# Optimization experiments

Measured on AMD Instinct MI355X. Metric: run time of the kernel, lower is better.

The kernel has to match this reference:

```python
import jax, jax.numpy as jnp
import numpy as np

B, N, C = 8, 4096, 768
H = 12
D = C // H            # 64
BN = C // 2           # bottleneck dim 384
EPS_LN = 1e-5
EPS_ATTN = 1e-6


def layer_norm(x, g, b):
    mu = jnp.mean(x, axis=-1, keepdims=True)
    var = jnp.mean(jnp.square(x - mu), axis=-1, keepdims=True)
    return (x - mu) * jax.lax.rsqrt(var + EPS_LN) * g + b


def setup_inputs() -> dict:
    key = jax.random.key(0)
    ks = jax.random.split(key, 8)
    s = 0.02
    return {
        "x": jax.random.normal(ks[0], (B, N, C), jnp.float32),
        "w_qkv": jax.random.normal(ks[1], (C, 3 * C), jnp.float32) * s,
        "b_qkv": jnp.zeros((3 * C,), jnp.float32),
        "w_proj": jax.random.normal(ks[2], (C, C), jnp.float32) * s,
        "b_proj": jnp.zeros((C,), jnp.float32),
        "g1": jnp.ones((C,), jnp.float32),
        "beta1": jnp.zeros((C,), jnp.float32),
        "g2": jnp.ones((C,), jnp.float32),
        "beta2": jnp.zeros((C,), jnp.float32),
        "w_down": jax.random.normal(ks[3], (C, BN), jnp.float32) * s,
        "b_down": jnp.zeros((BN,), jnp.float32),
        "w_up": jax.random.normal(ks[4], (BN, C), jnp.float32) * s,
        "b_up": jnp.zeros((C,), jnp.float32),
        "g3": jnp.ones((C,), jnp.float32),
        "beta3": jnp.zeros((C,), jnp.float32),
    }


def _linear_attention(x, w_qkv, b_qkv, w_proj, b_proj):
    # x: (B, N, C)
    qkv = x @ w_qkv + b_qkv                       # (B, N, 3C)
    qkv = qkv.reshape(B, N, 3, H, D)
    qkv = jnp.transpose(qkv, (2, 0, 3, 1, 4))     # (3, B, H, N, D)
    q, k, v = qkv[0], qkv[1], qkv[2]
    fm = lambda t: jax.nn.elu(t) + 1.0            # positive feature map
    q, k = fm(q), fm(k)
    kv = jnp.einsum('bhnd,bhnv->bhdv', k, v)      # (B, H, D, D)
    out = jnp.einsum('bhnd,bhdv->bhnv', q, kv)    # (B, H, N, D)
    k_sum = k.sum(axis=2)                         # (B, H, D)
    normalizer = jnp.einsum('bhnd,bhd->bhn', q, k_sum) + EPS_ATTN
    out = out / normalizer[..., None]
    out = jnp.transpose(out, (0, 2, 1, 3)).reshape(B, N, C)
    return out @ w_proj + b_proj


def reference(x, w_qkv, b_qkv, w_proj, b_proj, g1, beta1, g2, beta2,
              w_down, b_down, w_up, b_up, g3, beta3):
    # DinomalyBlock forward (eval mode: dropout/noise disabled)
    x = x + _linear_attention(layer_norm(x, g1, beta1), w_qkv, b_qkv, w_proj, b_proj)
    r = layer_norm(x, g2, beta2)
    h = jax.nn.gelu(r @ w_down + b_down, approximate=False)  # torch GELU default = exact
    h = h @ w_up + b_up
    return layer_norm(r + h, g3, beta3)
```

## Files before the change

kernel.cpp:

```cpp
#include <hip/hip_runtime.h>
#include <hip/hip_bf16.h>
#include <cstdio>


typedef __attribute__((ext_vector_type(8))) short short8;
typedef __attribute__((ext_vector_type(4))) float floatx4;

__device__ __forceinline__ float bf2f(unsigned short u) {
    return __uint_as_float(((unsigned int)u) << 16);
}
__device__ __forceinline__ unsigned short f2bf(float f) {
    __hip_bfloat16 h = __float2bfloat16(f);
    return *reinterpret_cast<unsigned short*>(&h);
}

__device__ __forceinline__ void async_copy16(const unsigned short* g, unsigned short* l) {
    __builtin_amdgcn_global_load_lds(
        (const __attribute__((address_space(1))) unsigned int*)g,
        (__attribute__((address_space(3))) unsigned int*)l, 16, 0, 0);
}

__device__ __forceinline__ floatx4 MFMA16(short8 a, short8 b, floatx4 c) {
    return __builtin_amdgcn_mfma_f32_16x16x32_bf16(a, b, c, 0, 0, 0);
}

__global__ __launch_bounds__(256) void transpose_all(
    const float* __restrict__ wq, const float* __restrict__ wp,
    const float* __restrict__ wd, const float* __restrict__ wu,
    unsigned short* __restrict__ tq, unsigned short* __restrict__ tp,
    unsigned short* __restrict__ td, unsigned short* __restrict__ tu)
{
    int blk = blockIdx.x;
    const float* w; unsigned short* o; int K, Nc, tx32;
    if (blk < 1728)      { w = wq; o = tq; K = 768; Nc = 2304; tx32 = 24; }
    else if (blk < 2304) { w = wp; o = tp; K = 768; Nc = 768;  tx32 = 24; blk -= 1728; }
    else if (blk < 2592) { w = wd; o = td; K = 768; Nc = 384;  tx32 = 24; blk -= 2304; }
    else                 { w = wu; o = tu; K = 384; Nc = 768;  tx32 = 12; blk -= 2592; }
    int kb = (blk % tx32) * 32, nb = (blk / tx32) * 32;
    __shared__ float tile[32][33];
    int tx = threadIdx.x & 31, ty = threadIdx.x >> 5;
    #pragma unroll
    for (int i = 0; i < 32; i += 8)
        tile[ty + i][tx] = w[(size_t)(kb + ty + i) * Nc + nb + tx];
    __syncthreads();
    #pragma unroll
    for (int i = 0; i < 32; i += 8)
        o[(size_t)(nb + ty + i) * K + kb + tx] = f2bf(tile[tx][ty + i]);
}

template<bool OBF16>
__global__ __launch_bounds__(384) void ln_kernel(
    const float* __restrict__ in, const float* __restrict__ gw,
    const float* __restrict__ bw, void* __restrict__ outp)
{
    int row = blockIdx.x;
    int t = threadIdx.x;
    float2 xv = ((const float2*)(in + (size_t)row * 768))[t];
    float s = xv.x + xv.y;
    float ss = xv.x * xv.x + xv.y * xv.y;
    #pragma unroll
    for (int o = 32; o > 0; o >>= 1) {
        s += __shfl_down(s, o);
        ss += __shfl_down(ss, o);
    }
    __shared__ float red[14];
    int wave = t >> 6, lane = t & 63;
    if (lane == 0) { red[wave] = s; red[6 + wave] = ss; }
    __syncthreads();
    if (t == 0) {
        float S = 0.f, SS = 0.f;
        #pragma unroll
        for (int i = 0; i < 6; i++) { S += red[i]; SS += red[6 + i]; }
        float mu = S * (1.0f / 768.0f);
        float var = SS * (1.0f / 768.0f) - mu * mu;
        red[12] = mu;
        red[13] = rsqrtf(var + 1e-5f);
    }
    __syncthreads();
    float mu = red[12], rstd = red[13];
    float2 g = ((const float2*)gw)[t];
    float2 b = ((const float2*)bw)[t];
    float y0 = (xv.x - mu) * rstd * g.x + b.x;
    float y1 = (xv.y - mu) * rstd * g.y + b.y;
    if (OBF16) {
        unsigned int pk = (unsigned int)f2bf(y0) | ((unsigned int)f2bf(y1) << 16);
        ((unsigned int*)outp)[(size_t)row * 384 + t] = pk;
    } else {
        ((float2*)outp)[(size_t)row * 384 + t] = make_float2(y0, y1);
    }
}

template<bool RES_F32, bool OUT_F32>
__global__ __launch_bounds__(384) void add_ln_kernel(
    const unsigned short* __restrict__ y, const void* __restrict__ resv,
    const float* __restrict__ gw, const float* __restrict__ bw,
    void* __restrict__ outp)
{
    int row = blockIdx.x;
    int t = threadIdx.x;
    unsigned int yp = ((const unsigned int*)(y + (size_t)row * 768))[t];
    float a0 = bf2f((unsigned short)(yp & 0xffff));
    float a1 = bf2f((unsigned short)(yp >> 16));
    float r0, r1;
    if (RES_F32) {
        float2 rv = ((const float2*)((const float*)resv + (size_t)row * 768))[t];
        r0 = rv.x; r1 = rv.y;
    } else {
        unsigned int rp = ((const unsigned int*)((const unsigned short*)resv + (size_t)row * 768))[t];
        r0 = bf2f((unsigned short)(rp & 0xffff));
        r1 = bf2f((unsigned short)(rp >> 16));
    }
    float v0 = a0 + r0, v1 = a1 + r1;
    float s = v0 + v1;
    float ss = v0 * v0 + v1 * v1;
    #pragma unroll
    for (int o = 32; o > 0; o >>= 1) {
        s += __shfl_down(s, o);
        ss += __shfl_down(ss, o);
    }
    __shared__ float red[14];
    int wave = t >> 6, lane = t & 63;
    if (lane == 0) { red[wave] = s; red[6 + wave] = ss; }
    __syncthreads();
    if (t == 0) {
        float S = 0.f, SS = 0.f;
        #pragma unroll
        for (int i = 0; i < 6; i++) { S += red[i]; SS += red[6 + i]; }
        float mu = S * (1.0f / 768.0f);
        float var = SS * (1.0f / 768.0f) - mu * mu;
        red[12] = mu;
        red[13] = rsqrtf(var + 1e-5f);
    }
    __syncthreads();
    float mu = red[12], rstd = red[13];
    float2 g = ((const float2*)gw)[t];
    float2 b = ((const float2*)bw)[t];
    float y0 = (v0 - mu) * rstd * g.x + b.x;
    float y1 = (v1 - mu) * rstd * g.y + b.y;
    if (OUT_F32) {
        ((float2*)outp)[(size_t)row * 384 + t] = make_float2(y0, y1);
    } else {
        unsigned int pk = (unsigned int)f2bf(y0) | ((unsigned int)f2bf(y1) << 16);
        ((unsigned int*)outp)[(size_t)row * 384 + t] = pk;
    }
}

template<int MODE>
__global__ __launch_bounds__(256, 4) void gemm_kernel(
    const unsigned short* __restrict__ A,
    const unsigned short* __restrict__ Wt,
    const float* __restrict__ bias,
    unsigned short* __restrict__ outp,
    int M, int K, int Nc)
{
    __shared__ __align__(16) unsigned short As[128][64];
    __shared__ __align__(16) unsigned short Bs[128][64];

    const int gx = gridDim.x;
    const int gy = gridDim.y;
    int rb, cb;
    {
        const int lid = blockIdx.y * gx + blockIdx.x;
        const int xcd = lid & 7;
        const int o   = lid >> 3;
        const int pry = gy >> 3;
        const int cpg = (gx >= 12) ? (gx >> 1) : gx;
        const int per = pry * cpg;
        const int grp = o / per;
        const int o2  = o - grp * per;
        rb = xcd * pry + o2 / cpg;
        cb = grp * cpg + o2 % cpg;
    }
    const int row0 = rb * 128;
    const int col0 = cb * 128;

    const int t = threadIdx.x;
    const int lane = t & 63;
    const int wave = t >> 6;
    const int wm = (wave >> 1) * 64;
    const int wn = (wave & 1) * 64;
    const int frow = lane & 15;
    const int quad = lane >> 4;
    const int lrow = lane >> 3;
    const int lchunk = (lane & 7) ^ lrow;

    floatx4 acc[4][4];
    #pragma unroll
    for (int i = 0; i < 4; i++)
        #pragma unroll
        for (int j = 0; j < 4; j++)
            acc[i][j] = (floatx4){0.f, 0.f, 0.f, 0.f};

    for (int k0 = 0; k0 < K; k0 += 64) {
        __syncthreads();
        #pragma unroll
        for (int q = 0; q < 4; q++) {
            int r = wave * 32 + q * 8 + lrow;
            async_copy16(A  + (size_t)(row0 + r) * K + k0 + lchunk * 8, &As[wave * 32 + q * 8][0]);
            async_copy16(Wt + (size_t)(col0 + r) * K + k0 + lchunk * 8, &Bs[wave * 32 + q * 8][0]);
        }
        __syncthreads();
        #pragma unroll
        for (int ks = 0; ks < 2; ks++) {
            const int pc = ((ks * 4 + quad) ^ (frow & 7)) * 8;
            short8 af[4], bf4[4];
            #pragma unroll
            for (int i = 0; i < 4; i++) af[i] = *(const short8*)&As[wm + i * 16 + frow][pc];
            #pragma unroll
            for (int j = 0; j < 4; j++) bf4[j] = *(const short8*)&Bs[wn + j * 16 + frow][pc];
            #pragma unroll
            for (int i = 0; i < 4; i++)
                #pragma unroll
                for (int j = 0; j < 4; j++)
                    acc[i][j] = MFMA16(af[i], bf4[j], acc[i][j]);
        }
    }

    #pragma unroll
    for (int i = 0; i < 4; i++) {
        #pragma unroll
        for (int j = 0; j < 4; j++) {
            int col = col0 + wn + j * 16 + frow;
            float bcol = bias[col];
            #pragma unroll
            for (int rr = 0; rr < 4; rr++) {
                int row = row0 + wm + i * 16 + quad * 4 + rr;
                float v = acc[i][j][rr] + bcol;
                if (MODE == 0) {
                    if (col < 1536) v = (v > 0.f) ? (v + 1.f) : expf(v);
                } else if (MODE == 2) {
                    v = 0.5f * v * (1.0f + erff(v * 0.70710678118654752f));
                }
                outp[(size_t)row * Nc + col] = f2bf(v);
            }
        }
    }
}

__global__ __launch_bounds__(256, 4) void kv_accum(
    const unsigned short* __restrict__ qkv, float* __restrict__ kvbuf)
{
    int blk = blockIdx.x;
    int chunk = blk & 7;
    int bh = blk >> 3;
    int b = bh / 12, h = bh % 12;
    int n0 = chunk * 512;
    int t = threadIdx.x;
    int d = t & 63, g = t >> 6;
    __shared__ float kl[32][68];
    __shared__ float vl[32][68];
    float kv[16];
    #pragma unroll
    for (int j = 0; j < 16; j++) kv[j] = 0.f;
    float ks = 0.f;

    int sr = t >> 3;
    int c16 = (t & 7) * 16;
    bool isk = c16 < 64;
    int cc = isk ? c16 : c16 - 64;
    const unsigned short* gbase =
        qkv + (size_t)(b * 4096 + n0 + sr) * 2304 + (isk ? 768 : 1536) + h * 64 + cc;
    uint4 r0, r1;
    auto loadg = [&](int nb) {
        const uint4* s = (const uint4*)(gbase + (size_t)nb * 2304);
        r0 = s[0]; r1 = s[1];
    };
    auto storel = [&]() {
        float* dst = isk ? &kl[sr][cc] : &vl[sr][cc];
        const unsigned short* u0 = (const unsigned short*)&r0;
        const unsigned short* u1 = (const unsigned short*)&r1;
        #pragma unroll
        for (int i = 0; i < 8; i++) dst[i] = bf2f(u0[i]);
        #pragma unroll
        for (int i = 0; i < 8; i++) dst[8 + i] = bf2f(u1[i]);
    };

    loadg(0);
    for (int c = 0; c < 16; c++) {
        storel();
        __syncthreads();
        if (c < 15) loadg((c + 1) * 32);
        #pragma unroll 8
        for (int r2 = 0; r2 < 32; r2++) {
            float kd = kl[r2][d];
            ks += kd;
            const float4* vv = (const float4*)&vl[r2][g * 16];
            float4 a0 = vv[0], a1 = vv[1], a2 = vv[2], a3 = vv[3];
            kv[0]  += kd * a0.x; kv[1]  += kd * a0.y; kv[2]  += kd * a0.z; kv[3]  += kd * a0.w;
            kv[4]  += kd * a1.x; kv[5]  += kd * a1.y; kv[6]  += kd * a1.z; kv[7]  += kd * a1.w;
            kv[8]  += kd * a2.x; kv[9]  += kd * a2.y; kv[10] += kd * a2.z; kv[11] += kd * a2.w;
            kv[12] += kd * a3.x; kv[13] += kd * a3.y; kv[14] += kd * a3.z; kv[15] += kd * a3.w;
        }
        __syncthreads();
    }
    float* dstg = kvbuf + (size_t)bh * 4160;
    #pragma unroll
    for (int j = 0; j < 16; j++)
        atomicAdd(&dstg[(g * 16 + j) * 64 + d], kv[j]);
    if (g == 0) atomicAdd(&dstg[4096 + d], ks);
}

__global__ __launch_bounds__(256) void attn_apply(
    const unsigned short* __restrict__ qkv, const float* __restrict__ kvbuf,
    unsigned short* __restrict__ attnC)
{
    int blk = blockIdx.x;
    int nchunk = blk & 31;
    int bh = blk >> 5;
    int b = bh / 12, h = bh % 12;
    int n0 = nchunk * 128;
    int t = threadIdx.x;
    int lane = t & 63, wave = t >> 6;
    __shared__ __align__(16) unsigned short ql[128][72];
    __shared__ __align__(16) unsigned short Bs[80][72];

    {
        const float* kvg = kvbuf + (size_t)bh * 4160;
        int e = t >> 2, d0 = (t & 3) * 16;
        const float4* src4 = (const float4*)(kvg + e * 64 + d0);
        #pragma unroll
        for (int i = 0; i < 4; i++) {
            float4 v = src4[i];
            unsigned long long pk = (unsigned long long)f2bf(v.x)
                | ((unsigned long long)f2bf(v.y) << 16)
                | ((unsigned long long)f2bf(v.z) << 32)
                | ((unsigned long long)f2bf(v.w) << 48);
            *(unsigned long long*)&Bs[e][d0 + i * 4] = pk;
        }
        if (t < 64) {
            Bs[64][t] = f2bf(kvg[4096 + t]);
            #pragma unroll
            for (int r = 65; r < 80; r++) Bs[r][t] = 0;
        }
    }
    {
        int r = t >> 1, c0 = (t & 1) * 32;
        const uint4* src = (const uint4*)(qkv + (size_t)(b * 4096 + n0 + r) * 2304 + h * 64 + c0);
        uint4* dst = (uint4*)&ql[r][c0];
        #pragma unroll
        for (int i = 0; i < 4; i++) dst[i] = src[i];
    }
    __syncthreads();

    int frow = lane & 15, quad = lane >> 4;
    floatx4 acc[2][5];
    #pragma unroll
    for (int it = 0; it < 2; it++)
        #pragma unroll
        for (int jt = 0; jt < 5; jt++)
            acc[it][jt] = (floatx4){0.f, 0.f, 0.f, 0.f};

    #pragma unroll
    for (int ks = 0; ks < 2; ks++) {
        int fk = ks * 32 + quad * 8;
        short8 a0 = *(const short8*)&ql[wave * 32 + frow][fk];
        short8 a1 = *(const short8*)&ql[wave * 32 + 16 + frow][fk];
        #pragma unroll
        for (int jt = 0; jt < 5; jt++) {
            short8 bb = *(const short8*)&Bs[jt * 16 + frow][fk];
            acc[0][jt] = __builtin_amdgcn_mfma_f32_16x16x32_bf16(a0, bb, acc[0][jt], 0, 0, 0);
            acc[1][jt] = __builtin_amdgcn_mfma_f32_16x16x32_bf16(a1, bb, acc[1][jt], 0, 0, 0);
        }
    }

    #pragma unroll
    for (int it = 0; it < 2; it++) {
        #pragma unroll
        for (int rr = 0; rr < 4; rr++) {
            float nv = __shfl(acc[it][4][rr], (lane & 48));
            float inv = 1.0f / (nv + 1e-6f);
            int row = n0 + wave * 32 + it * 16 + quad * 4 + rr;
            size_t obase = (size_t)(b * 4096 + row) * 768 + h * 64;
            #pragma unroll
            for (int jt = 0; jt < 4; jt++)
                attnC[obase + jt * 16 + frow] = f2bf(acc[it][jt][rr] * inv);
        }
    }
}

extern "C" void kernel_launch(void* const* d_in, const int* in_sizes, int n_in,
                              void* d_out, int out_size, void* d_ws, size_t ws_size,
                              hipStream_t stream)
{
    const float* x      = (const float*)d_in[0];
    const float* w_qkv  = (const float*)d_in[1];
    const float* b_qkv  = (const float*)d_in[2];
    const float* w_proj = (const float*)d_in[3];
    const float* b_proj = (const float*)d_in[4];
    const float* g1     = (const float*)d_in[5];
    const float* be1    = (const float*)d_in[6];
    const float* g2     = (const float*)d_in[7];
    const float* be2    = (const float*)d_in[8];
    const float* w_down = (const float*)d_in[9];
    const float* b_down = (const float*)d_in[10];
    const float* w_up   = (const float*)d_in[11];
    const float* b_up   = (const float*)d_in[12];
    const float* g3     = (const float*)d_in[13];
    const float* be3    = (const float*)d_in[14];

    char* p = (char*)d_ws;
    auto take = [&](size_t b) { char* q = p; p += (b + 255) & ~(size_t)255; return q; };
    unsigned short* wtq  = (unsigned short*)take((size_t)2304 * 768 * 2);
    unsigned short* wtp  = (unsigned short*)take((size_t)768 * 768 * 2);
    unsigned short* wtd  = (unsigned short*)take((size_t)384 * 768 * 2);
    unsigned short* wtu  = (unsigned short*)take((size_t)768 * 384 * 2);
    unsigned short* bufA = (unsigned short*)take((size_t)32768 * 768 * 2);
    unsigned short* qkvb = (unsigned short*)take((size_t)32768 * 2304 * 2);
    float*          kvb  = (float*)take((size_t)96 * 4160 * 4);
    unsigned short* hbuf = (unsigned short*)take((size_t)32768 * 384 * 2);
    unsigned short* rbuf    = qkvb;
    unsigned short* projout = qkvb + (size_t)32768 * 768;
    unsigned short* upout   = qkvb + (size_t)2 * 32768 * 768;

    size_t needed = (size_t)(p - (char*)d_ws);
    if (needed > ws_size)
        fprintf(stderr, "WARNING: ws too small: need %zu have %zu\n", needed, ws_size);

    transpose_all<<<2880, 256, 0, stream>>>(w_qkv, w_proj, w_down, w_up, wtq, wtp, wtd, wtu);
    hipMemsetAsync(kvb, 0, (size_t)96 * 4160 * 4, stream);

    ln_kernel<true><<<32768, 384, 0, stream>>>(x, g1, be1, bufA);
    gemm_kernel<0><<<dim3(18, 256), 256, 0, stream>>>(bufA, wtq, b_qkv, qkvb, 32768, 768, 2304);
    kv_accum<<<768, 256, 0, stream>>>(qkvb, kvb);
    attn_apply<<<3072, 256, 0, stream>>>(qkvb, kvb, bufA);
    gemm_kernel<1><<<dim3(6, 256), 256, 0, stream>>>(bufA, wtp, b_proj, projout, 32768, 768, 768);
    add_ln_kernel<true, false><<<32768, 384, 0, stream>>>(projout, x, g2, be2, rbuf);
    gemm_kernel<2><<<dim3(3, 256), 256, 0, stream>>>(rbuf, wtd, b_down, hbuf, 32768, 768, 384);
    gemm_kernel<1><<<dim3(6, 256), 256, 0, stream>>>(hbuf, wtu, b_up, upout, 32768, 384, 768);
    add_ln_kernel<false, true><<<32768, 384, 0, stream>>>(upout, rbuf, g3, be3, (float*)d_out);
}
```

Baseline: 649.1 us.

## Process two rows per LayerNorm block with float4 loads; drop GEMM block swizzle

The LayerNorm and add+LayerNorm kernels now handle two rows per 384-thread block, each thread loading four elements with float4 or uint2 accesses, which halves the block count and widens the memory transactions. Separately, the GEMM kernel drops its XCD-aware block-index remapping and uses plain blockIdx tiling. The wider loads should cut per-block overhead in the bandwidth-bound LN kernels. Removing the swizzle may hurt L2 locality for the GEMMs on the multi-XCD chip.

After: 646.6 us. Within noise of the previous version (-0.4%).

```diff
diff --git a/kernel.cpp b/kernel.cpp
--- a/kernel.cpp
+++ b/kernel.cpp
@@ -53,40 +53,46 @@
     const float* __restrict__ in, const float* __restrict__ gw,
     const float* __restrict__ bw, void* __restrict__ outp)
 {
-    int row = blockIdx.x;
     int t = threadIdx.x;
-    float2 xv = ((const float2*)(in + (size_t)row * 768))[t];
-    float s = xv.x + xv.y;
-    float ss = xv.x * xv.x + xv.y * xv.y;
+    int half = (t >= 192) ? 1 : 0;
+    int tt = t - half * 192;
+    int row = blockIdx.x * 2 + half;
+    float4 xv = ((const float4*)(in + (size_t)row * 768))[tt];
+    float s = xv.x + xv.y + xv.z + xv.w;
+    float ss = xv.x * xv.x + xv.y * xv.y + xv.z * xv.z + xv.w * xv.w;
     #pragma unroll
     for (int o = 32; o > 0; o >>= 1) {
         s += __shfl_down(s, o);
         ss += __shfl_down(ss, o);
     }
-    __shared__ float red[14];
+    __shared__ float red[16];
     int wave = t >> 6, lane = t & 63;
-    if (lane == 0) { red[wave] = s; red[6 + wave] = ss; }
-    __syncthreads();
-    if (t == 0) {
-        float S = 0.f, SS = 0.f;
-        #pragma unroll
-        for (int i = 0; i < 6; i++) { S += red[i]; SS += red[6 + i]; }
+    if (lane == 0) { red[wave] = s; red[8 + wave] = ss; }
+    __syncthreads();
+    if (tt == 0) {
+        int w0 = half * 3;
+        float S = red[w0] + red[w0 + 1] + red[w0 + 2];
+        float SS = red[8 + w0] + red[8 + w0 + 1] + red[8 + w0 + 2];
         float mu = S * (1.0f / 768.0f);
         float var = SS * (1.0f / 768.0f) - mu * mu;
-        red[12] = mu;
-        red[13] = rsqrtf(var + 1e-5f);
-    }
-    __syncthreads();
-    float mu = red[12], rstd = red[13];
-    float2 g = ((const float2*)gw)[t];
-    float2 b = ((const float2*)bw)[t];
+        red[6 + half] = mu;
+        red[14 + half] = rsqrtf(var + 1e-5f);
+    }
+    __syncthreads();
+    float mu = red[6 + half], rstd = red[14 + half];
+    float4 g = ((const float4*)gw)[tt];
+    float4 b = ((const float4*)bw)[tt];
     float y0 = (xv.x - mu) * rstd * g.x + b.x;
     float y1 = (xv.y - mu) * rstd * g.y + b.y;
+    float y2 = (xv.z - mu) * rstd * g.z + b.z;
+    float y3 = (xv.w - mu) * rstd * g.w + b.w;
     if (OBF16) {
-        unsigned int pk = (unsigned int)f2bf(y0) | ((unsigned int)f2bf(y1) << 16);
-        ((unsigned int*)outp)[(size_t)row * 384 + t] = pk;
+        uint2 pk;
+        pk.x = (unsigned int)f2bf(y0) | ((unsigned int)f2bf(y1) << 16);
+        pk.y = (unsigned int)f2bf(y2) | ((unsigned int)f2bf(y3) << 16);
+        ((uint2*)outp)[(size_t)row * 192 + tt] = pk;
     } else {
-        ((float2*)outp)[(size_t)row * 384 + t] = make_float2(y0, y1);
+        ((float4*)outp)[(size_t)row * 192 + tt] = make_float4(y0, y1, y2, y3);
     }
 }
 
@@ -96,52 +102,62 @@
     const float* __restrict__ gw, const float* __restrict__ bw,
     void* __restrict__ outp)
 {
-    int row = blockIdx.x;
     int t = threadIdx.x;
-    unsigned int yp = ((const unsigned int*)(y + (size_t)row * 768))[t];
-    float a0 = bf2f((unsigned short)(yp & 0xffff));
-    float a1 = bf2f((unsigned short)(yp >> 16));
-    float r0, r1;
+    int half = (t >= 192) ? 1 : 0;
+    int tt = t - half * 192;
+    int row = blockIdx.x * 2 + half;
+    uint2 yp = ((const uint2*)(y + (size_t)row * 768))[tt];
+    float a0 = bf2f((unsigned short)(yp.x & 0xffff));
+    float a1 = bf2f((unsigned short)(yp.x >> 16));
+    float a2 = bf2f((unsigned short)(yp.y & 0xffff));
+    float a3 = bf2f((unsigned short)(yp.y >> 16));
+    float r0, r1, r2, r3;
     if (RES_F32) {
-        float2 rv = ((const float2*)((const float*)resv + (size_t)row * 768))[t];
-        r0 = rv.x; r1 = rv.y;
+        float4 rv = ((const float4*)((const float*)resv + (size_t)row * 768))[tt];
+        r0 = rv.x; r1 = rv.y; r2 = rv.z; r3 = rv.w;
     } else {
-        unsigned int rp = ((const unsigned int*)((const unsigned short*)resv + (size_t)row * 768))[t];
-        r0 = bf2f((unsigned short)(rp & 0xffff));
-        r1 = bf2f((unsigned short)(rp >> 16));
-    }
-    float v0 = a0 + r0, v1 = a1 + r1;
-    float s = v0 + v1;
-    float ss = v0 * v0 + v1 * v1;
+        uint2 rp = ((const uint2*)((const unsigned short*)resv + (size_t)row * 768))[tt];
+        r0 = bf2f((unsigned short)(rp.x & 0xffff));
+        r1 = bf2f((unsigned short)(rp.x >> 16));
+        r2 = bf2f((unsigned short)(rp.y & 0xffff));
+        r3 = bf2f((unsigned short)(rp.y >> 16));
+    }
+    float v0 = a0 + r0, v1 = a1 + r1, v2 = a2 + r2, v3 = a3 + r3;
+    float s = v0 + v1 + v2 + v3;
+    float ss = v0 * v0 + v1 * v1 + v2 * v2 + v3 * v3;
     #pragma unroll
     for (int o = 32; o > 0; o >>= 1) {
         s += __shfl_down(s, o);
         ss += __shfl_down(ss, o);
     }
-    __shared__ float red[14];
+    __shared__ float red[16];
     int wave = t >> 6, lane = t & 63;
-    if (lane == 0) { red[wave] = s; red[6 + wave] = ss; }
-    __syncthreads();
-    if (t == 0) {
-        float S = 0.f, SS = 0.f;
-        #pragma unroll
-        for (int i = 0; i < 6; i++) { S += red[i]; SS += red[6 + i]; }
+    if (lane == 0) { red[wave] = s; red[8 + wave] = ss; }
+    __syncthreads();
+    if (tt == 0) {
+        int w0 = half * 3;
+        float S = red[w0] + red[w0 + 1] + red[w0 + 2];
+        float SS = red[8 + w0] + red[8 + w0 + 1] + red[8 + w0 + 2];
         float mu = S * (1.0f / 768.0f);
         float var = SS * (1.0f / 768.0f) - mu * mu;
-        red[12] = mu;
-        red[13] = rsqrtf(var + 1e-5f);
-    }
-    __syncthreads();
-    float mu = red[12], rstd = red[13];
-    float2 g = ((const float2*)gw)[t];
-    float2 b = ((const float2*)bw)[t];
+        red[6 + half] = mu;
+        red[14 + half] = rsqrtf(var + 1e-5f);
+    }
+    __syncthreads();
+    float mu = red[6 + half], rstd = red[14 + half];
+    float4 g = ((const float4*)gw)[tt];
+    float4 b = ((const float4*)bw)[tt];
     float y0 = (v0 - mu) * rstd * g.x + b.x;
     float y1 = (v1 - mu) * rstd * g.y + b.y;
+    float y2 = (v2 - mu) * rstd * g.z + b.z;
+    float y3 = (v3 - mu) * rstd * g.w + b.w;
     if (OUT_F32) {
-        ((float2*)outp)[(size_t)row * 384 + t] = make_float2(y0, y1);
+        ((float4*)outp)[(size_t)row * 192 + tt] = make_float4(y0, y1, y2, y3);
     } else {
-        unsigned int pk = (unsigned int)f2bf(y0) | ((unsigned int)f2bf(y1) << 16);
-        ((unsigned int*)outp)[(size_t)row * 384 + t] = pk;
+        uint2 pk;
+        pk.x = (unsigned int)f2bf(y0) | ((unsigned int)f2bf(y1) << 16);
+        pk.y = (unsigned int)f2bf(y2) | ((unsigned int)f2bf(y3) << 16);
+        ((uint2*)outp)[(size_t)row * 192 + tt] = pk;
     }
 }
 
@@ -155,25 +171,8 @@
 {
     __shared__ __align__(16) unsigned short As[128][64];
     __shared__ __align__(16) unsigned short Bs[128][64];
-
-    const int gx = gridDim.x;
-    const int gy = gridDim.y;
-    int rb, cb;
-    {
-        const int lid = blockIdx.y * gx + blockIdx.x;
-        const int xcd = lid & 7;
-        const int o   = lid >> 3;
-        const int pry = gy >> 3;
-        const int cpg = (gx >= 12) ? (gx >> 1) : gx;
-        const int per = pry * cpg;
-        const int grp = o / per;
-        const int o2  = o - grp * per;
-        rb = xcd * pry + o2 / cpg;
-        cb = grp * cpg + o2 % cpg;
-    }
-    const int row0 = rb * 128;
-    const int col0 = cb * 128;
-
+    const int row0 = blockIdx.y * 128;
+    const int col0 = blockIdx.x * 128;
     const int t = threadIdx.x;
     const int lane = t & 63;
     const int wave = t >> 6;
@@ -419,13 +418,13 @@
     transpose_all<<<2880, 256, 0, stream>>>(w_qkv, w_proj, w_down, w_up, wtq, wtp, wtd, wtu);
     hipMemsetAsync(kvb, 0, (size_t)96 * 4160 * 4, stream);
 
-    ln_kernel<true><<<32768, 384, 0, stream>>>(x, g1, be1, bufA);
+    ln_kernel<true><<<16384, 384, 0, stream>>>(x, g1, be1, bufA);
     gemm_kernel<0><<<dim3(18, 256), 256, 0, stream>>>(bufA, wtq, b_qkv, qkvb, 32768, 768, 2304);
     kv_accum<<<768, 256, 0, stream>>>(qkvb, kvb);
     attn_apply<<<3072, 256, 0, stream>>>(qkvb, kvb, bufA);
     gemm_kernel<1><<<dim3(6, 256), 256, 0, stream>>>(bufA, wtp, b_proj, projout, 32768, 768, 768);
-    add_ln_kernel<true, false><<<32768, 384, 0, stream>>>(projout, x, g2, be2, rbuf);
+    add_ln_kernel<true, false><<<16384, 384, 0, stream>>>(projout, x, g2, be2, rbuf);
     gemm_kernel<2><<<dim3(3, 256), 256, 0, stream>>>(rbuf, wtd, b_down, hbuf, 32768, 768, 384);
     gemm_kernel<1><<<dim3(6, 256), 256, 0, stream>>>(hbuf, wtu, b_up, upout, 32768, 384, 768);
-    add_ln_kernel<false, true><<<32768, 384, 0, stream>>>(upout, rbuf, g3, be3, (float*)d_out);
-}
+    add_ln_kernel<false, true><<<16384, 384, 0, stream>>>(upout, rbuf, g3, be3, (float*)d_out);
+}
```

## Use wave-per-row layernorms, drop GEMM XCD swizzle, stage attention output via LDS

Applied to the files above, without the earlier changes.

The layernorm and add-layernorm kernels now assign one wavefront per row, with four rows per 256-thread block. They use float4/uint2 vector loads and a shuffle-xor reduction, so the LDS round trip and both block barriers go away. The GEMM drops its XCD-aware block remapping and uses plain blockIdx tiling, which may reduce L2 locality across chiplets. The attention-apply epilogue writes results into LDS first and then stores them with coalesced 16-byte global writes instead of scattered 2-byte stores.

New measurement: 611.9 us. -5.7%, faster.

```diff
diff --git a/kernel.cpp b/kernel.cpp
--- a/kernel.cpp
+++ b/kernel.cpp
@@ -49,99 +49,127 @@
 }
 
 template<bool OBF16>
-__global__ __launch_bounds__(384) void ln_kernel(
+__global__ __launch_bounds__(256) void ln_kernel(
     const float* __restrict__ in, const float* __restrict__ gw,
     const float* __restrict__ bw, void* __restrict__ outp)
 {
-    int row = blockIdx.x;
     int t = threadIdx.x;
-    float2 xv = ((const float2*)(in + (size_t)row * 768))[t];
-    float s = xv.x + xv.y;
-    float ss = xv.x * xv.x + xv.y * xv.y;
-    #pragma unroll
-    for (int o = 32; o > 0; o >>= 1) {
-        s += __shfl_down(s, o);
-        ss += __shfl_down(ss, o);
-    }
-    __shared__ float red[14];
-    int wave = t >> 6, lane = t & 63;
-    if (lane == 0) { red[wave] = s; red[6 + wave] = ss; }
-    __syncthreads();
-    if (t == 0) {
-        float S = 0.f, SS = 0.f;
-        #pragma unroll
-        for (int i = 0; i < 6; i++) { S += red[i]; SS += red[6 + i]; }
-        float mu = S * (1.0f / 768.0f);
-        float var = SS * (1.0f / 768.0f) - mu * mu;
-        red[12] = mu;
-        red[13] = rsqrtf(var + 1e-5f);
-    }
-    __syncthreads();
-    float mu = red[12], rstd = red[13];
-    float2 g = ((const float2*)gw)[t];
-    float2 b = ((const float2*)bw)[t];
-    float y0 = (xv.x - mu) * rstd * g.x + b.x;
-    float y1 = (xv.y - mu) * rstd * g.y + b.y;
+    int lane = t & 63, wave = t >> 6;
+    int row = blockIdx.x * 4 + wave;
+    const float4* src = (const float4*)(in + (size_t)row * 768);
+    float4 x0 = src[lane], x1 = src[lane + 64], x2 = src[lane + 128];
+    float s  = (x0.x + x0.y + x0.z + x0.w)
+             + (x1.x + x1.y + x1.z + x1.w)
+             + (x2.x + x2.y + x2.z + x2.w);
+    float ss = (x0.x * x0.x + x0.y * x0.y + x0.z * x0.z + x0.w * x0.w)
+             + (x1.x * x1.x + x1.y * x1.y + x1.z * x1.z + x1.w * x1.w)
+             + (x2.x * x2.x + x2.y * x2.y + x2.z * x2.z + x2.w * x2.w);
+    #pragma unroll
+    for (int o = 1; o < 64; o <<= 1) {
+        s += __shfl_xor(s, o);
+        ss += __shfl_xor(ss, o);
+    }
+    float mu = s * (1.0f / 768.0f);
+    float var = ss * (1.0f / 768.0f) - mu * mu;
+    float rstd = rsqrtf(var + 1e-5f);
+    float4 g0 = ((const float4*)gw)[lane], g1 = ((const float4*)gw)[lane + 64],
+           g2 = ((const float4*)gw)[lane + 128];
+    float4 b0 = ((const float4*)bw)[lane], b1 = ((const float4*)bw)[lane + 64],
+           b2 = ((const float4*)bw)[lane + 128];
+    float4 y0, y1, y2;
+    y0.x = (x0.x - mu) * rstd * g0.x + b0.x; y0.y = (x0.y - mu) * rstd * g0.y + b0.y;
+    y0.z = (x0.z - mu) * rstd * g0.z + b0.z; y0.w = (x0.w - mu) * rstd * g0.w + b0.w;
+    y1.x = (x1.x - mu) * rstd * g1.x + b1.x; y1.y = (x1.y - mu) * rstd * g1.y + b1.y;
+    y1.z = (x1.z - mu) * rstd * g1.z + b1.z; y1.w = (x1.w - mu) * rstd * g1.w + b1.w;
+    y2.x = (x2.x - mu) * rstd * g2.x + b2.x; y2.y = (x2.y - mu) * rstd * g2.y + b2.y;
+    y2.z = (x2.z - mu) * rstd * g2.z + b2.z; y2.w = (x2.w - mu) * rstd * g2.w + b2.w;
     if (OBF16) {
-        unsigned int pk = (unsigned int)f2bf(y0) | ((unsigned int)f2bf(y1) << 16);
-        ((unsigned int*)outp)[(size_t)row * 384 + t] = pk;
+        uint2* dst = (uint2*)outp + (size_t)row * 192;
+        uint2 p0, p1, p2;
+        p0.x = (unsigned int)f2bf(y0.x) | ((unsigned int)f2bf(y0.y) << 16);
+        p0.y = (unsigned int)f2bf(y0.z) | ((unsigned int)f2bf(y0.w) << 16);
+        p1.x = (unsigned int)f2bf(y1.x) | ((unsigned int)f2bf(y1.y) << 16);
+        p1.y = (unsigned int)f2bf(y1.z) | ((unsigned int)f2bf(y1.w) << 16);
+        p2.x = (unsigned int)f2bf(y2.x) | ((unsigned int)f2bf(y2.y) << 16);
+        p2.y = (unsigned int)f2bf(y2.z) | ((unsigned int)f2bf(y2.w) << 16);
+        dst[lane] = p0; dst[lane + 64] = p1; dst[lane + 128] = p2;
     } else {
-        ((float2*)outp)[(size_t)row * 384 + t] = make_float2(y0, y1);
+        float4* dst = (float4*)outp + (size_t)row * 192;
+        dst[lane] = y0; dst[lane + 64] = y1; dst[lane + 128] = y2;
     }
 }
 
 template<bool RES_F32, bool OUT_F32>
-__global__ __launch_bounds__(384) void add_ln_kernel(
+__global__ __launch_bounds__(256) void add_ln_kernel(
     const unsigned short* __restrict__ y, const void* __restrict__ resv,
     const float* __restrict__ gw, const float* __restrict__ bw,
     void* __restrict__ outp)
 {
-    int row = blockIdx.x;
     int t = threadIdx.x;
-    unsigned int yp = ((const unsigned int*)(y + (size_t)row * 768))[t];
-    float a0 = bf2f((unsigned short)(yp & 0xffff));
-    float a1 = bf2f((unsigned short)(yp >> 16));
-    float r0, r1;
+    int lane = t & 63, wave = t >> 6;
+    int row = blockIdx.x * 4 + wave;
+    const uint2* ysrc = (const uint2*)(y + (size_t)row * 768);
+    uint2 ya = ysrc[lane], yb = ysrc[lane + 64], yc = ysrc[lane + 128];
+    float v[12];
+    v[0] = bf2f((unsigned short)(ya.x & 0xffff)); v[1] = bf2f((unsigned short)(ya.x >> 16));
+    v[2] = bf2f((unsigned short)(ya.y & 0xffff)); v[3] = bf2f((unsigned short)(ya.y >> 16));
+    v[4] = bf2f((unsigned short)(yb.x & 0xffff)); v[5] = bf2f((unsigned short)(yb.x >> 16));
+    v[6] = bf2f((unsigned short)(yb.y & 0xffff)); v[7] = bf2f((unsigned short)(yb.y >> 16));
+    v[8] = bf2f((unsigned short)(yc.x & 0xffff)); v[9] = bf2f((unsigned short)(yc.x >> 16));
+    v[10] = bf2f((unsigned short)(yc.y & 0xffff)); v[11] = bf2f((unsigned short)(yc.y >> 16));
     if (RES_F32) {
-        float2 rv = ((const float2*)((const float*)resv + (size_t)row * 768))[t];
-        r0 = rv.x; r1 = rv.y;
+        const float4* rsrc = (const float4*)((const float*)resv + (size_t)row * 768);
+        float4 r0 = rsrc[lane], r1 = rsrc[lane + 64], r2 = rsrc[lane + 128];
+        v[0] += r0.x; v[1] += r0.y; v[2] += r0.z; v[3] += r0.w;
+        v[4] += r1.x; v[5] += r1.y; v[6] += r1.z; v[7] += r1.w;
+        v[8] += r2.x; v[9] += r2.y; v[10] += r2.z; v[11] += r2.w;
     } else {
-        unsigned int rp = ((const unsigned int*)((const unsigned short*)resv + (size_t)row * 768))[t];
-        r0 = bf2f((unsigned short)(rp & 0xffff));
-        r1 = bf2f((unsigned short)(rp >> 16));
-    }
-    float v0 = a0 + r0, v1 = a1 + r1;
-    float s = v0 + v1;
-    float ss = v0 * v0 + v1 * v1;
-    #pragma unroll
-    for (int o = 32; o > 0; o >>= 1) {
-        s += __shfl_down(s, o);
-        ss += __shfl_down(ss, o);
-    }
-    __shared__ float red[14];
-    int wave = t >> 6, lane = t & 63;
-    if (lane == 0) { red[wave] = s; red[6 + wave] = ss; }
-    __syncthreads();
-    if (t == 0) {
-        float S = 0.f, SS = 0.f;
-        #pragma unroll
-        for (int i = 0; i < 6; i++) { S += red[i]; SS += red[6 + i]; }
-        float mu = S * (1.0f / 768.0f);
-        float var = SS * (1.0f / 768.0f) - mu * mu;
-        red[12] = mu;
-        red[13] = rsqrtf(var + 1e-5f);
-    }
-    __syncthreads();
-    float mu = red[12], rstd = red[13];
-    float2 g = ((const float2*)gw)[t];
-    float2 b = ((const float2*)bw)[t];
-    float y0 = (v0 - mu) * rstd * g.x + b.x;
-    float y1 = (v1 - mu) * rstd * g.y + b.y;
+        const uint2* rsrc = (const uint2*)((const unsigned short*)resv + (size_t)row * 768);
+        uint2 r0 = rsrc[lane], r1 = rsrc[lane + 64], r2 = rsrc[lane + 128];
+        v[0] += bf2f((unsigned short)(r0.x & 0xffff)); v[1] += bf2f((unsigned short)(r0.x >> 16));
+        v[2] += bf2f((unsigned short)(r0.y & 0xffff)); v[3] += bf2f((unsigned short)(r0.y >> 16));
+        v[4] += bf2f((unsigned short)(r1.x & 0xffff)); v[5] += bf2f((unsigned short)(r1.x >> 16));
+        v[6] += bf2f((unsigned short)(r1.y & 0xffff)); v[7] += bf2f((unsigned short)(r1.y >> 16));
+        v[8] += bf2f((unsigned short)(r2.x & 0xffff)); v[9] += bf2f((unsigned short)(r2.x >> 16));
+        v[10] += bf2f((unsigned short)(r2.y & 0xffff)); v[11] += bf2f((unsigned short)(r2.y >> 16));
+    }
+    float s = 0.f, ss = 0.f;
+    #pragma unroll
+    for (int i = 0; i < 12; i++) { s += v[i]; ss += v[i] * v[i]; }
+    #pragma unroll
+    for (int o = 1; o < 64; o <<= 1) {
+        s += __shfl_xor(s, o);
+        ss += __shfl_xor(ss, o);
+    }
+    float mu = s * (1.0f / 768.0f);
+    float var = ss * (1.0f / 768.0f) - mu * mu;
+    float rstd = rsqrtf(var + 1e-5f);
+    float4 g0 = ((const float4*)gw)[lane], g1 = ((const float4*)gw)[lane + 64],
+           g2 = ((const float4*)gw)[lane + 128];
+    float4 b0 = ((const float4*)bw)[lane], b1 = ((const float4*)bw)[lane + 64],
+           b2 = ((const float4*)bw)[lane + 128];
+    float yv[12];
+    yv[0] = (v[0] - mu) * rstd * g0.x + b0.x; yv[1] = (v[1] - mu) * rstd * g0.y + b0.y;
+    yv[2] = (v[2] - mu) * rstd * g0.z + b0.z; yv[3] = (v[3] - mu) * rstd * g0.w + b0.w;
+    yv[4] = (v[4] - mu) * rstd * g1.x + b1.x; yv[5] = (v[5] - mu) * rstd * g1.y + b1.y;
+    yv[6] = (v[6] - mu) * rstd * g1.z + b1.z; yv[7] = (v[7] - mu) * rstd * g1.w + b1.w;
+    yv[8] = (v[8] - mu) * rstd * g2.x + b2.x; yv[9] = (v[9] - mu) * rstd * g2.y + b2.y;
+    yv[10] = (v[10] - mu) * rstd * g2.z + b2.z; yv[11] = (v[11] - mu) * rstd * g2.w + b2.w;
     if (OUT_F32) {
-        ((float2*)outp)[(size_t)row * 384 + t] = make_float2(y0, y1);
+        float4* dst = (float4*)outp + (size_t)row * 192;
+        dst[lane] = make_float4(yv[0], yv[1], yv[2], yv[3]);
+        dst[lane + 64] = make_float4(yv[4], yv[5], yv[6], yv[7]);
+        dst[lane + 128] = make_float4(yv[8], yv[9], yv[10], yv[11]);
     } else {
-        unsigned int pk = (unsigned int)f2bf(y0) | ((unsigned int)f2bf(y1) << 16);
-        ((unsigned int*)outp)[(size_t)row * 384 + t] = pk;
+        uint2* dst = (uint2*)outp + (size_t)row * 192;
+        uint2 p0, p1, p2;
+        p0.x = (unsigned int)f2bf(yv[0]) | ((unsigned int)f2bf(yv[1]) << 16);
+        p0.y = (unsigned int)f2bf(yv[2]) | ((unsigned int)f2bf(yv[3]) << 16);
+        p1.x = (unsigned int)f2bf(yv[4]) | ((unsigned int)f2bf(yv[5]) << 16);
+        p1.y = (unsigned int)f2bf(yv[6]) | ((unsigned int)f2bf(yv[7]) << 16);
+        p2.x = (unsigned int)f2bf(yv[8]) | ((unsigned int)f2bf(yv[9]) << 16);
+        p2.y = (unsigned int)f2bf(yv[10]) | ((unsigned int)f2bf(yv[11]) << 16);
+        dst[lane] = p0; dst[lane + 64] = p1; dst[lane + 128] = p2;
     }
 }
 
@@ -155,25 +183,8 @@
 {
     __shared__ __align__(16) unsigned short As[128][64];
     __shared__ __align__(16) unsigned short Bs[128][64];
-
-    const int gx = gridDim.x;
-    const int gy = gridDim.y;
-    int rb, cb;
-    {
-        const int lid = blockIdx.y * gx + blockIdx.x;
-        const int xcd = lid & 7;
-        const int o   = lid >> 3;
-        const int pry = gy >> 3;
-        const int cpg = (gx >= 12) ? (gx >> 1) : gx;
-        const int per = pry * cpg;
-        const int grp = o / per;
-        const int o2  = o - grp * per;
-        rb = xcd * pry + o2 / cpg;
-        cb = grp * cpg + o2 % cpg;
-    }
-    const int row0 = rb * 128;
-    const int col0 = cb * 128;
-
+    const int row0 = blockIdx.y * 128;
+    const int col0 = blockIdx.x * 128;
     const int t = threadIdx.x;
     const int lane = t & 63;
     const int wave = t >> 6;
@@ -369,12 +380,20 @@
         for (int rr = 0; rr < 4; rr++) {
             float nv = __shfl(acc[it][4][rr], (lane & 48));
             float inv = 1.0f / (nv + 1e-6f);
-            int row = n0 + wave * 32 + it * 16 + quad * 4 + rr;
-            size_t obase = (size_t)(b * 4096 + row) * 768 + h * 64;
+            int lr = it * 16 + quad * 4 + rr;
             #pragma unroll
             for (int jt = 0; jt < 4; jt++)
-                attnC[obase + jt * 16 + frow] = f2bf(acc[it][jt][rr] * inv);
-        }
+                ql[wave * 32 + lr][jt * 16 + frow] = f2bf(acc[it][jt][rr] * inv);
+        }
+    }
+    #pragma unroll
+    for (int j = 0; j < 4; j++) {
+        int u = j * 64 + lane;
+        int lr = u >> 3;
+        int c8 = (u & 7) * 8;
+        uint4 val = *(const uint4*)&ql[wave * 32 + lr][c8];
+        int row = n0 + wave * 32 + lr;
+        *(uint4*)&attnC[(size_t)(b * 4096 + row) * 768 + h * 64 + c8] = val;
     }
 }
 
@@ -419,13 +438,13 @@
     transpose_all<<<2880, 256, 0, stream>>>(w_qkv, w_proj, w_down, w_up, wtq, wtp, wtd, wtu);
     hipMemsetAsync(kvb, 0, (size_t)96 * 4160 * 4, stream);
 
-    ln_kernel<true><<<32768, 384, 0, stream>>>(x, g1, be1, bufA);
+    ln_kernel<true><<<8192, 256, 0, stream>>>(x, g1, be1, bufA);
     gemm_kernel<0><<<dim3(18, 256), 256, 0, stream>>>(bufA, wtq, b_qkv, qkvb, 32768, 768, 2304);
     kv_accum<<<768, 256, 0, stream>>>(qkvb, kvb);
     attn_apply<<<3072, 256, 0, stream>>>(qkvb, kvb, bufA);
     gemm_kernel<1><<<dim3(6, 256), 256, 0, stream>>>(bufA, wtp, b_proj, projout, 32768, 768, 768);
-    add_ln_kernel<true, false><<<32768, 384, 0, stream>>>(projout, x, g2, be2, rbuf);
+    add_ln_kernel<true, false><<<8192, 256, 0, stream>>>(projout, x, g2, be2, rbuf);
     gemm_kernel<2><<<dim3(3, 256), 256, 0, stream>>>(rbuf, wtd, b_down, hbuf, 32768, 768, 384);
     gemm_kernel<1><<<dim3(6, 256), 256, 0, stream>>>(hbuf, wtu, b_up, upout, 32768, 384, 768);
-    add_ln_kernel<false, true><<<32768, 384, 0, stream>>>(upout, rbuf, g3, be3, (float*)d_out);
-}
+    add_ln_kernel<false, true><<<8192, 256, 0, stream>>>(upout, rbuf, g3, be3, (float*)d_out);
+}
```
